# Optimization experiments

Measured on AMD Instinct MI355X. Metric: run time of the kernel, lower is better.

Reference implementation:

```python
import jax, jax.numpy as jnp
import numpy as np

N_NODES = 100_000
N_EDGES = 1_600_000
D_IN, D_H, D_OUT = 128, 128, 64


def setup_inputs() -> dict:
    key = jax.random.key(0)
    ks = jax.random.split(key, 8)
    x = jax.random.normal(ks[0], (N_NODES, D_IN), dtype=jnp.float32)
    edge_index = jax.random.randint(ks[1], (2, N_EDGES), 0, N_NODES, dtype=jnp.int32)
    def glorot(k, shape):
        lim = float(np.sqrt(6.0 / (shape[0] + shape[1])))
        return jax.random.uniform(k, shape, jnp.float32, -lim, lim)
    return {
        "x": x,
        "edge_index": edge_index,
        "W1": glorot(ks[2], (D_IN, D_H)),  "b1": jnp.zeros((D_H,), jnp.float32),
        "W2": glorot(ks[3], (D_H, D_H)),   "b2": jnp.zeros((D_H,), jnp.float32),
        "W3": glorot(ks[4], (D_H, D_OUT)), "b3": jnp.zeros((D_OUT,), jnp.float32),
    }


def gcn_conv(x, edge_index, W, b, num_nodes):
    # PyG GCNConv: add self-loops, symmetric D^-1/2 (A+I) D^-1/2 normalization,
    # linear transform before aggregation, then bias.
    xw = x @ W                                   # [N, D_out]
    loops = jnp.arange(num_nodes, dtype=edge_index.dtype)
    row = jnp.concatenate([edge_index[0], loops])  # source nodes
    col = jnp.concatenate([edge_index[1], loops])  # target nodes
    deg = jax.ops.segment_sum(jnp.ones_like(col, xw.dtype), col,
                              num_segments=num_nodes)
    dinv = jnp.where(deg > 0, jax.lax.rsqrt(jnp.maximum(deg, 1e-12)), 0.0)
    norm = dinv[row] * dinv[col]                 # [E+N]
    msg = xw[row] * norm[:, None]                # gather + scale
    out = jax.ops.segment_sum(msg, col, num_segments=num_nodes)
    return out + b


def reference(x, edge_index, W1, b1, W2, b2, W3, b3):
    # Dropout(0.2) is identity in eval/inference mode.
    h = jax.nn.relu(gcn_conv(x, edge_index, W1, b1, N_NODES))
    h = jax.nn.relu(gcn_conv(h, edge_index, W2, b2, N_NODES))
    return gcn_conv(h, edge_index, W3, b3, N_NODES)
```

## Files before the change

kernel.cpp:

```cpp
#include <hip/hip_runtime.h>

#define NN 100000
#define NE 1600000
constexpr int KDIM = 128;
constexpr int NPB = 128;
constexpr int G = (NN + NPB - 1) / NPB;
constexpr int CH = 4096;
constexpr int NCH = (NE + CH - 1) / CH;
constexpr int CAP = 4000;

typedef _Float16 f16x4 __attribute__((ext_vector_type(4)));
typedef _Float16 f16x8 __attribute__((ext_vector_type(8)));
typedef float f32x4 __attribute__((ext_vector_type(4)));
using half8 = f16x8;

__device__ __forceinline__ int swz(int byte) {
  return byte ^ (((byte >> 8) & 7) << 4);
}


__global__ __launch_bounds__(256) void k_zero(int* p, int n) {
  int i = blockIdx.x * 256 + threadIdx.x;
  if (i < n) p[i] = 0;
}

__global__ __launch_bounds__(256) void k_bucketP(const int* __restrict__ row,
                                                 const int* __restrict__ col,
                                                 int* __restrict__ cursor,
                                                 unsigned long long* __restrict__ temp) {
  __shared__ int h[G];
  for (int i = threadIdx.x; i < G; i += 256) h[i] = 0;
  __syncthreads();
  const int base = blockIdx.x * CH;
  const int m = min(CH, NE - base);
  for (int i = threadIdx.x; i < m; i += 256) atomicAdd(&h[col[base + i] >> 7], 1);
  __syncthreads();
  for (int i = threadIdx.x; i < G; i += 256) {
    int c = h[i];
    if (c) h[i] = atomicAdd(&cursor[i], c);
  }
  __syncthreads();
  for (int i = threadIdx.x; i < m; i += 256) {
    int cc = col[base + i];
    int rr = row[base + i];
    int slot = atomicAdd(&h[cc >> 7], 1);
    temp[(size_t)(cc >> 7) * CAP + slot] =
        ((unsigned long long)(unsigned)cc << 32) | (unsigned)rr;
  }
}

__global__ void k_bscan(const int* __restrict__ cnt, int* __restrict__ bbase) {
  __shared__ int sd[256];
  const int t = threadIdx.x;
  int v[4];
  int s = 0;
#pragma unroll
  for (int j = 0; j < 4; ++j) {
    int idx = t * 4 + j;
    v[j] = (idx < G) ? cnt[idx] : 0;
    s += v[j];
  }
  sd[t] = s;
  __syncthreads();
  for (int off = 1; off < 256; off <<= 1) {
    int x = (t >= off) ? sd[t - off] : 0;
    __syncthreads();
    sd[t] += x;
    __syncthreads();
  }
  int run = sd[t] - s;
#pragma unroll
  for (int j = 0; j < 4; ++j) {
    int idx = t * 4 + j;
    if (idx < G) bbase[idx] = run;
    run += v[j];
  }
  if (t == 255) bbase[G] = run;
}

__global__ __launch_bounds__(256) void k_groupP(const unsigned long long* __restrict__ temp,
                                                const int* __restrict__ bbase,
                                                int* __restrict__ rowptr,
                                                float* __restrict__ dinv,
                                                int* __restrict__ srcs) {
  __shared__ int fill[NPB];
  __shared__ int nbase[NPB];
  __shared__ int sc[NPB];
  const int g = blockIdx.x, t = threadIdx.x;
  const int lo = g * NPB;
  const int b0 = bbase[g];
  const int n = bbase[g + 1] - b0;
  const unsigned long long* tp = temp + (size_t)g * CAP;
  if (t < NPB) fill[t] = 0;
  __syncthreads();
  for (int s = t; s < n; s += 256) {
    int cc = (int)(tp[s] >> 32);
    atomicAdd(&fill[cc & (NPB - 1)], 1);
  }
  __syncthreads();
  int v = 0;
  if (t < NPB) {
    v = fill[t];
    sc[t] = v;
  }
  __syncthreads();
  for (int off = 1; off < NPB; off <<= 1) {
    int x = 0;
    if (t < NPB && t >= off) x = sc[t - off];
    __syncthreads();
    if (t < NPB) sc[t] += x;
    __syncthreads();
  }
  if (t < NPB) {
    int excl = sc[t] - v;
    nbase[t] = b0 + excl;
    int node = lo + t;
    if (node < NN) {
      rowptr[node] = b0 + excl;
      dinv[node] = rsqrtf((float)(v + 1));
    }
    fill[t] = 0;
  }
  if (g == G - 1 && t == 0) rowptr[NN] = NE;
  __syncthreads();
  for (int s = t; s < n; s += 256) {
    unsigned long long p = tp[s];
    int cc = (int)(p >> 32);
    int rr = (int)(unsigned)(p & 0xffffffffull);
    int c = cc & (NPB - 1);
    int slot = atomicAdd(&fill[c], 1);
    srcs[nbase[c] + slot] = rr;
  }
}

__global__ __launch_bounds__(256) void k_wconvAll(const float* __restrict__ W1,
                                                  const float* __restrict__ W2,
                                                  const float* __restrict__ W3,
                                                  _Float16* __restrict__ w1h,
                                                  _Float16* __restrict__ w2h,
                                                  _Float16* __restrict__ w3h) {
  int i = blockIdx.x * 256 + threadIdx.x;
  if (i < 16384) {
    int k = i >> 7, c = i & 127;
    w1h[c * 128 + k] = (_Float16)W1[i];
  } else if (i < 32768) {
    int j = i - 16384;
    int k = j >> 7, c = j & 127;
    w2h[c * 128 + k] = (_Float16)W2[j];
  } else if (i < 40960) {
    int j = i - 32768;
    int k = j >> 6, c = j & 63;
    w3h[c * 128 + k] = (_Float16)W3[j];
  }
}

template <int BN, bool F32IN>
__global__ __launch_bounds__(256, 2) void k_gemm_mfma(const void* __restrict__ Ain,
                                                      const _Float16* __restrict__ Wt_g,
                                                      const float* __restrict__ dinv,
                                                      _Float16* __restrict__ Y, int M) {
  constexpr int NB = BN / 16;
  __shared__ _Float16 Ah[128 * 128];
  __shared__ _Float16 Wt[BN * 128];
  const int t = threadIdx.x;
  const int rbase = blockIdx.x * 128;

  for (int c = t; c < BN * 16; c += 256) {
    f16x8 v = *(const f16x8*)((const char*)Wt_g + c * 16);
    *(f16x8*)((char*)Wt + swz(c * 16)) = v;
  }
  if constexpr (F32IN) {
    const float* A = (const float*)Ain;
    for (int c = t; c < 2048; c += 256) {
      int r = c >> 4, kc = c & 15;
      int row = rbase + r;
      f16x8 h = {};
      if (row < M) {
        float dv = dinv[row];
        const float* p = A + (size_t)row * 128 + kc * 8;
        float4 u0 = *(const float4*)p;
        float4 u1 = *(const float4*)(p + 4);
        h[0] = (_Float16)(u0.x * dv);
        h[1] = (_Float16)(u0.y * dv);
        h[2] = (_Float16)(u0.z * dv);
        h[3] = (_Float16)(u0.w * dv);
        h[4] = (_Float16)(u1.x * dv);
        h[5] = (_Float16)(u1.y * dv);
        h[6] = (_Float16)(u1.z * dv);
        h[7] = (_Float16)(u1.w * dv);
      }
      *(f16x8*)((char*)Ah + swz(c * 16)) = h;
    }
  } else {
    const _Float16* A = (const _Float16*)Ain;
    for (int c = t; c < 2048; c += 256) {
      int r = c >> 4;
      int row = rbase + r;
      f16x8 h = {};
      if (row < M) h = *(const f16x8*)(A + (size_t)row * 128 + (c & 15) * 8);
      *(f16x8*)((char*)Ah + swz(c * 16)) = h;
    }
  }
  __syncthreads();

  const int wave = t >> 6, lane = t & 63;
  const int l16 = lane & 15, lk = lane >> 4;

  f32x4 acc[2][NB];
#pragma unroll
  for (int mm = 0; mm < 2; ++mm)
#pragma unroll
    for (int n = 0; n < NB; ++n) acc[mm][n] = (f32x4){0.f, 0.f, 0.f, 0.f};

#pragma unroll
  for (int ks = 0; ks < 4; ++ks) {
    const int kbyte = ks * 64 + lk * 16;
    f16x8 afr[2];
#pragma unroll
    for (int mm = 0; mm < 2; ++mm) {
      int row = wave * 32 + mm * 16 + l16;
      afr[mm] = *(const f16x8*)((const char*)Ah + swz(row * 256 + kbyte));
    }
#pragma unroll
    for (int n = 0; n < NB; ++n) {
      int wrow = n * 16 + l16;
      f16x8 wfr = *(const f16x8*)((const char*)Wt + swz(wrow * 256 + kbyte));
#pragma unroll
      for (int mm = 0; mm < 2; ++mm)
        acc[mm][n] = __builtin_amdgcn_mfma_f32_16x16x32_f16(wfr, afr[mm], acc[mm][n], 0, 0, 0);
    }
  }

#pragma unroll
  for (int mm = 0; mm < 2; ++mm) {
    int row = rbase + wave * 32 + mm * 16 + l16;
    if (row < M) {
      _Float16* yr = Y + (size_t)row * BN + lk * 4;
#pragma unroll
      for (int n = 0; n < NB; ++n) {
        f16x4 h = {(_Float16)acc[mm][n][0], (_Float16)acc[mm][n][1],
                   (_Float16)acc[mm][n][2], (_Float16)acc[mm][n][3]};
        *(f16x4*)(yr + n * 16) = h;
      }
    } else if (row == M) {
      _Float16* yr = Y + (size_t)row * BN + lk * 4;
      f16x4 z = {};
#pragma unroll
      for (int n = 0; n < NB; ++n) *(f16x4*)(yr + n * 16) = z;
    }
  }
}

__global__ __launch_bounds__(256) void k_agg128h(const _Float16* __restrict__ Y,
                                                 const int* __restrict__ rowptr,
                                                 const int* __restrict__ srcs,
                                                 const float* __restrict__ dinv,
                                                 const float* __restrict__ bias,
                                                 _Float16* __restrict__ Out, int n) {
  const int wave = threadIdx.x >> 6;
  const int lane = threadIdx.x & 63;
  const int node = blockIdx.x * 4 + wave;
  if (node >= n) return;
  const int part = lane >> 4;
  const int q = lane & 15;
  const int jb = rowptr[node];
  const int je = rowptr[node + 1];

  float acc[8];
#pragma unroll
  for (int j = 0; j < 8; ++j) acc[j] = 0.f;
  {
    half8 s = *(const half8*)(Y + (size_t)node * 128 + q * 8);
    if (part == 0) {
#pragma unroll
      for (int j = 0; j < 8; ++j) acc[j] = (float)s[j];
    }
  }

  for (int j0 = jb; j0 < je; j0 += 64) {
    const int m = min(64, je - j0);
    const int idx = (lane < m) ? srcs[j0 + lane] : NN;
    for (int eb = 0; eb < m; eb += 32) {
      const int e0 = eb + part;
      int s0 = __shfl(idx, e0);
      int s1 = __shfl(idx, e0 + 4);
      int s2 = __shfl(idx, e0 + 8);
      int s3 = __shfl(idx, e0 + 12);
      int s4 = __shfl(idx, e0 + 16);
      int s5 = __shfl(idx, e0 + 20);
      int s6 = __shfl(idx, e0 + 24);
      int s7 = __shfl(idx, e0 + 28);
      half8 v0 = *(const half8*)(Y + (size_t)s0 * 128 + q * 8);
      half8 v1 = *(const half8*)(Y + (size_t)s1 * 128 + q * 8);
      half8 v2 = *(const half8*)(Y + (size_t)s2 * 128 + q * 8);
      half8 v3 = *(const half8*)(Y + (size_t)s3 * 128 + q * 8);
      half8 v4 = *(const half8*)(Y + (size_t)s4 * 128 + q * 8);
      half8 v5 = *(const half8*)(Y + (size_t)s5 * 128 + q * 8);
      half8 v6 = *(const half8*)(Y + (size_t)s6 * 128 + q * 8);
      half8 v7 = *(const half8*)(Y + (size_t)s7 * 128 + q * 8);
      half8 sA = (v0 + v1) + (v2 + v3);
      half8 sB = (v4 + v5) + (v6 + v7);
#pragma unroll
      for (int j = 0; j < 8; ++j) acc[j] += (float)sA[j];
#pragma unroll
      for (int j = 0; j < 8; ++j) acc[j] += (float)sB[j];
    }
  }

#pragma unroll
  for (int j = 0; j < 8; ++j) {
    acc[j] += __shfl_xor(acc[j], 16);
    acc[j] += __shfl_xor(acc[j], 32);
  }

  if (part == 0) {
    const float dv = dinv[node];
    f16x8 h;
#pragma unroll
    for (int j = 0; j < 8; ++j) {
      float o = fmaf(acc[j], dv, bias[q * 8 + j]);
      o = fmaxf(o, 0.f);
      h[j] = (_Float16)(o * dv);
    }
    *(f16x8*)(Out + (size_t)node * 128 + q * 8) = h;
  }
}

__global__ __launch_bounds__(256) void k_agg64h(const _Float16* __restrict__ Y,
                                                const int* __restrict__ rowptr,
                                                const int* __restrict__ srcs,
                                                const float* __restrict__ dinv,
                                                const float* __restrict__ bias,
                                                float* __restrict__ Out, int n) {
  const int wave = threadIdx.x >> 6;
  const int lane = threadIdx.x & 63;
  const int node = blockIdx.x * 4 + wave;
  if (node >= n) return;
  const int part = lane >> 3;
  const int q = lane & 7;
  const int jb = rowptr[node];
  const int je = rowptr[node + 1];

  float acc[8];
#pragma unroll
  for (int j = 0; j < 8; ++j) acc[j] = 0.f;
  {
    half8 s = *(const half8*)(Y + (size_t)node * 64 + q * 8);
    if (part == 0) {
#pragma unroll
      for (int j = 0; j < 8; ++j) acc[j] = (float)s[j];
    }
  }

  for (int j0 = jb; j0 < je; j0 += 64) {
    const int m = min(64, je - j0);
    const int idx = (lane < m) ? srcs[j0 + lane] : NN;
    const int e0 = part;
    int s0 = __shfl(idx, e0);
    int s1 = __shfl(idx, e0 + 8);
    int s2 = __shfl(idx, e0 + 16);
    int s3 = __shfl(idx, e0 + 24);
    int s4 = __shfl(idx, e0 + 32);
    int s5 = __shfl(idx, e0 + 40);
    int s6 = __shfl(idx, e0 + 48);
    int s7 = __shfl(idx, e0 + 56);
    half8 v0 = *(const half8*)(Y + (size_t)s0 * 64 + q * 8);
    half8 v1 = *(const half8*)(Y + (size_t)s1 * 64 + q * 8);
    half8 v2 = *(const half8*)(Y + (size_t)s2 * 64 + q * 8);
    half8 v3 = *(const half8*)(Y + (size_t)s3 * 64 + q * 8);
    half8 v4 = *(const half8*)(Y + (size_t)s4 * 64 + q * 8);
    half8 v5 = *(const half8*)(Y + (size_t)s5 * 64 + q * 8);
    half8 v6 = *(const half8*)(Y + (size_t)s6 * 64 + q * 8);
    half8 v7 = *(const half8*)(Y + (size_t)s7 * 64 + q * 8);
    half8 sA = (v0 + v1) + (v2 + v3);
    half8 sB = (v4 + v5) + (v6 + v7);
#pragma unroll
    for (int j = 0; j < 8; ++j) acc[j] += (float)sA[j];
#pragma unroll
    for (int j = 0; j < 8; ++j) acc[j] += (float)sB[j];
  }

#pragma unroll
  for (int j = 0; j < 8; ++j) {
    acc[j] += __shfl_xor(acc[j], 8);
    acc[j] += __shfl_xor(acc[j], 16);
    acc[j] += __shfl_xor(acc[j], 32);
  }

  if (part == 0) {
    const float dv = dinv[node];
    float o[8];
#pragma unroll
    for (int j = 0; j < 8; ++j) o[j] = fmaf(acc[j], dv, bias[q * 8 + j]);
    float* orow = Out + (size_t)node * 64 + q * 8;
    *(float4*)(orow) = make_float4(o[0], o[1], o[2], o[3]);
    *(float4*)(orow + 4) = make_float4(o[4], o[5], o[6], o[7]);
  }
}


extern "C" void kernel_launch(void* const* d_in, const int* in_sizes, int n_in,
                              void* d_out, int out_size, void* d_ws, size_t ws_size,
                              hipStream_t stream) {
  const float* x = (const float*)d_in[0];
  const int* ei = (const int*)d_in[1];
  const float* W1 = (const float*)d_in[2];
  const float* b1 = (const float*)d_in[3];
  const float* W2 = (const float*)d_in[4];
  const float* b2 = (const float*)d_in[5];
  const float* W3 = (const float*)d_in[6];
  const float* b3 = (const float*)d_in[7];
  float* out = (float*)d_out;

  const int* erow = ei;
  const int* ecol = ei + NE;

  char* w = (char*)d_ws;
  auto alloc = [&](size_t b) {
    char* p = w;
    w += (b + 255) & ~(size_t)255;
    return (void*)p;
  };
  float* dinv = (float*)alloc((size_t)NN * 4);
  int* rowptr = (int*)alloc((size_t)(NN + 1) * 4);
  int* cursor = (int*)alloc((size_t)G * 4);
  int* bbase = (int*)alloc((size_t)(G + 1) * 4);
  int* srcs = (int*)alloc((size_t)NE * 4);
  _Float16* w1h = (_Float16*)alloc((size_t)128 * 128 * 2);
  _Float16* w2h = (_Float16*)alloc((size_t)128 * 128 * 2);
  _Float16* w3h = (_Float16*)alloc((size_t)128 * 64 * 2);
  _Float16* ybuf = (_Float16*)alloc((size_t)(NN + 1) * 128 * 2);
  _Float16* hbuf = (_Float16*)alloc((size_t)(NN + 1) * 128 * 2);
  unsigned long long* temp = (unsigned long long*)ybuf;

  k_zero<<<(G + 255) / 256, 256, 0, stream>>>(cursor, G);
  k_bucketP<<<NCH, 256, 0, stream>>>(erow, ecol, cursor, temp);
  k_bscan<<<1, 256, 0, stream>>>(cursor, bbase);
  k_groupP<<<G, 256, 0, stream>>>(temp, bbase, rowptr, dinv, srcs);
  k_wconvAll<<<160, 256, 0, stream>>>(W1, W2, W3, w1h, w2h, w3h);

  const int nbG = (NN + 127) / 128;
  const int nbA = (NN + 3) / 4;

  k_gemm_mfma<128, true><<<nbG, 256, 0, stream>>>(x, w1h, dinv, ybuf, NN);
  k_agg128h<<<nbA, 256, 0, stream>>>(ybuf, rowptr, srcs, dinv, b1, hbuf, NN);
  k_gemm_mfma<128, false><<<nbG, 256, 0, stream>>>(hbuf, w2h, dinv, ybuf, NN);
  k_agg128h<<<nbA, 256, 0, stream>>>(ybuf, rowptr, srcs, dinv, b2, hbuf, NN);
  k_gemm_mfma<64, false><<<nbG, 256, 0, stream>>>(hbuf, w3h, dinv, ybuf, NN);
  k_agg64h<<<nbA, 256, 0, stream>>>(ybuf, rowptr, srcs, dinv, b3, out, NN);
}
```

Measured before the change: 279.1 us.

## Pack bucket entries to 32 bits, merge scan with weight convert, use global_load_lds

Bucket temp entries shrink from 64-bit (col,row) pairs to 32-bit words that pack a 7-bit local column with a 17-bit source row, halving scratch traffic in the bucket and group passes. The bucketing chunk size doubles. The bucket scan and the weight conversion now run in one launch instead of two. The GEMM loads W and full A tiles straight into LDS with global_load_lds, keeping the swizzle on the global side. The aggregation kernels load the self-loop row only in the lanes that use it.

```diff
diff --git a/kernel.cpp b/kernel.cpp
--- a/kernel.cpp
+++ b/kernel.cpp
@@ -5,10 +5,11 @@
 constexpr int KDIM = 128;
 constexpr int NPB = 128;
 constexpr int G = (NN + NPB - 1) / NPB;
-constexpr int CH = 4096;
+constexpr int CH = 8192;
 constexpr int NCH = (NE + CH - 1) / CH;
 constexpr int CAP = 4000;
 
+typedef unsigned int u32;
 typedef _Float16 f16x4 __attribute__((ext_vector_type(4)));
 typedef _Float16 f16x8 __attribute__((ext_vector_type(8)));
 typedef float f32x4 __attribute__((ext_vector_type(4)));
@@ -18,6 +19,12 @@
   return byte ^ (((byte >> 8) & 7) << 4);
 }
 
+__device__ __forceinline__ void gload16(const void* g, void* l) {
+  __builtin_amdgcn_global_load_lds(
+      (const __attribute__((address_space(1))) u32*)g,
+      (__attribute__((address_space(3))) u32*)l, 16, 0, 0);
+}
+
 
 __global__ __launch_bounds__(256) void k_zero(int* p, int n) {
   int i = blockIdx.x * 256 + threadIdx.x;
@@ -27,7 +34,7 @@
 __global__ __launch_bounds__(256) void k_bucketP(const int* __restrict__ row,
                                                  const int* __restrict__ col,
                                                  int* __restrict__ cursor,
-                                                 unsigned long long* __restrict__ temp) {
+                                                 u32* __restrict__ temp) {
   __shared__ int h[G];
   for (int i = threadIdx.x; i < G; i += 256) h[i] = 0;
   __syncthreads();
@@ -44,41 +51,63 @@
     int cc = col[base + i];
     int rr = row[base + i];
     int slot = atomicAdd(&h[cc >> 7], 1);
-    temp[(size_t)(cc >> 7) * CAP + slot] =
-        ((unsigned long long)(unsigned)cc << 32) | (unsigned)rr;
-  }
-}
-
-__global__ void k_bscan(const int* __restrict__ cnt, int* __restrict__ bbase) {
-  __shared__ int sd[256];
+    temp[(size_t)(cc >> 7) * CAP + slot] = ((u32)(cc & 127) << 17) | (u32)rr;
+  }
+}
+
+__global__ __launch_bounds__(256) void k_scan_wconv(const int* __restrict__ cnt,
+                                                    int* __restrict__ bbase,
+                                                    const float* __restrict__ W1,
+                                                    const float* __restrict__ W2,
+                                                    const float* __restrict__ W3,
+                                                    _Float16* __restrict__ w1h,
+                                                    _Float16* __restrict__ w2h,
+                                                    _Float16* __restrict__ w3h) {
   const int t = threadIdx.x;
-  int v[4];
-  int s = 0;
-#pragma unroll
-  for (int j = 0; j < 4; ++j) {
-    int idx = t * 4 + j;
-    v[j] = (idx < G) ? cnt[idx] : 0;
-    s += v[j];
-  }
-  sd[t] = s;
-  __syncthreads();
-  for (int off = 1; off < 256; off <<= 1) {
-    int x = (t >= off) ? sd[t - off] : 0;
+  if (blockIdx.x == 0) {
+    __shared__ int sd[256];
+    int v[4];
+    int s = 0;
+#pragma unroll
+    for (int j = 0; j < 4; ++j) {
+      int idx = t * 4 + j;
+      v[j] = (idx < G) ? cnt[idx] : 0;
+      s += v[j];
+    }
+    sd[t] = s;
     __syncthreads();
-    sd[t] += x;
-    __syncthreads();
-  }
-  int run = sd[t] - s;
-#pragma unroll
-  for (int j = 0; j < 4; ++j) {
-    int idx = t * 4 + j;
-    if (idx < G) bbase[idx] = run;
-    run += v[j];
-  }
-  if (t == 255) bbase[G] = run;
-}
-
-__global__ __launch_bounds__(256) void k_groupP(const unsigned long long* __restrict__ temp,
+    for (int off = 1; off < 256; off <<= 1) {
+      int x = (t >= off) ? sd[t - off] : 0;
+      __syncthreads();
+      sd[t] += x;
+      __syncthreads();
+    }
+    int run = sd[t] - s;
+#pragma unroll
+    for (int j = 0; j < 4; ++j) {
+      int idx = t * 4 + j;
+      if (idx < G) bbase[idx] = run;
+      run += v[j];
+    }
+    if (t == 255) bbase[G] = run;
+  } else {
+    int i = (blockIdx.x - 1) * 256 + t;
+    if (i < 16384) {
+      int k = i >> 7, c = i & 127;
+      w1h[c * 128 + k] = (_Float16)W1[i];
+    } else if (i < 32768) {
+      int j = i - 16384;
+      int k = j >> 7, c = j & 127;
+      w2h[c * 128 + k] = (_Float16)W2[j];
+    } else if (i < 40960) {
+      int j = i - 32768;
+      int k = j >> 6, c = j & 63;
+      w3h[c * 128 + k] = (_Float16)W3[j];
+    }
+  }
+}
+
+__global__ __launch_bounds__(256) void k_groupP(const u32* __restrict__ temp,
                                                 const int* __restrict__ bbase,
                                                 int* __restrict__ rowptr,
                                                 float* __restrict__ dinv,
@@ -90,13 +119,10 @@
   const int lo = g * NPB;
   const int b0 = bbase[g];
   const int n = bbase[g + 1] - b0;
-  const unsigned long long* tp = temp + (size_t)g * CAP;
+  const u32* tp = temp + (size_t)g * CAP;
   if (t < NPB) fill[t] = 0;
   __syncthreads();
-  for (int s = t; s < n; s += 256) {
-    int cc = (int)(tp[s] >> 32);
-    atomicAdd(&fill[cc & (NPB - 1)], 1);
-  }
+  for (int s = t; s < n; s += 256) atomicAdd(&fill[tp[s] >> 17], 1);
   __syncthreads();
   int v = 0;
   if (t < NPB) {
@@ -124,33 +150,10 @@
   if (g == G - 1 && t == 0) rowptr[NN] = NE;
   __syncthreads();
   for (int s = t; s < n; s += 256) {
-    unsigned long long p = tp[s];
-    int cc = (int)(p >> 32);
-    int rr = (int)(unsigned)(p & 0xffffffffull);
-    int c = cc & (NPB - 1);
+    u32 p = tp[s];
+    int c = p >> 17;
     int slot = atomicAdd(&fill[c], 1);
-    srcs[nbase[c] + slot] = rr;
-  }
-}
-
-__global__ __launch_bounds__(256) void k_wconvAll(const float* __restrict__ W1,
-                                                  const float* __restrict__ W2,
-                                                  const float* __restrict__ W3,
-                                                  _Float16* __restrict__ w1h,
-                                                  _Float16* __restrict__ w2h,
-                                                  _Float16* __restrict__ w3h) {
-  int i = blockIdx.x * 256 + threadIdx.x;
-  if (i < 16384) {
-    int k = i >> 7, c = i & 127;
-    w1h[c * 128 + k] = (_Float16)W1[i];
-  } else if (i < 32768) {
-    int j = i - 16384;
-    int k = j >> 7, c = j & 127;
-    w2h[c * 128 + k] = (_Float16)W2[j];
-  } else if (i < 40960) {
-    int j = i - 32768;
-    int k = j >> 6, c = j & 63;
-    w3h[c * 128 + k] = (_Float16)W3[j];
+    srcs[nbase[c] + slot] = (int)(p & 0x1FFFFu);
   }
 }
 
@@ -164,10 +167,15 @@
   __shared__ _Float16 Wt[BN * 128];
   const int t = threadIdx.x;
   const int rbase = blockIdx.x * 128;
-
-  for (int c = t; c < BN * 16; c += 256) {
-    f16x8 v = *(const f16x8*)((const char*)Wt_g + c * 16);
-    *(f16x8*)((char*)Wt + swz(c * 16)) = v;
+  const int wbase = (t & ~63) * 16;
+
+  {
+    const char* Wg = (const char*)Wt_g;
+    char* Wl = (char*)Wt;
+#pragma unroll
+    for (int c0 = 0; c0 < BN * 16; c0 += 256) {
+      gload16(Wg + swz((c0 + t) * 16), Wl + c0 * 16 + wbase);
+    }
   }
   if constexpr (F32IN) {
     const float* A = (const float*)Ain;
@@ -191,6 +199,13 @@
       }
       *(f16x8*)((char*)Ah + swz(c * 16)) = h;
     }
+  } else if (rbase + 128 <= M) {
+    const char* Ag = (const char*)Ain + (size_t)rbase * 256;
+    char* Al = (char*)Ah;
+#pragma unroll
+    for (int c0 = 0; c0 < 2048; c0 += 256) {
+      gload16(Ag + swz((c0 + t) * 16), Al + c0 * 16 + wbase);
+    }
   } else {
     const _Float16* A = (const _Float16*)Ain;
     for (int c = t; c < 2048; c += 256) {
@@ -269,12 +284,10 @@
   float acc[8];
 #pragma unroll
   for (int j = 0; j < 8; ++j) acc[j] = 0.f;
-  {
+  if (part == 0) {
     half8 s = *(const half8*)(Y + (size_t)node * 128 + q * 8);
-    if (part == 0) {
-#pragma unroll
-      for (int j = 0; j < 8; ++j) acc[j] = (float)s[j];
-    }
+#pragma unroll
+    for (int j = 0; j < 8; ++j) acc[j] = (float)s[j];
   }
 
   for (int j0 = jb; j0 < je; j0 += 64) {
@@ -344,12 +357,10 @@
   float acc[8];
 #pragma unroll
   for (int j = 0; j < 8; ++j) acc[j] = 0.f;
-  {
+  if (part == 0) {
     half8 s = *(const half8*)(Y + (size_t)node * 64 + q * 8);
-    if (part == 0) {
-#pragma unroll
-      for (int j = 0; j < 8; ++j) acc[j] = (float)s[j];
-    }
+#pragma unroll
+    for (int j = 0; j < 8; ++j) acc[j] = (float)s[j];
   }
 
   for (int j0 = jb; j0 < je; j0 += 64) {
@@ -431,13 +442,12 @@
   _Float16* w3h = (_Float16*)alloc((size_t)128 * 64 * 2);
   _Float16* ybuf = (_Float16*)alloc((size_t)(NN + 1) * 128 * 2);
   _Float16* hbuf = (_Float16*)alloc((size_t)(NN + 1) * 128 * 2);
-  unsigned long long* temp = (unsigned long long*)ybuf;
+  u32* temp = (u32*)ybuf;
 
   k_zero<<<(G + 255) / 256, 256, 0, stream>>>(cursor, G);
   k_bucketP<<<NCH, 256, 0, stream>>>(erow, ecol, cursor, temp);
-  k_bscan<<<1, 256, 0, stream>>>(cursor, bbase);
+  k_scan_wconv<<<161, 256, 0, stream>>>(cursor, bbase, W1, W2, W3, w1h, w2h, w3h);
   k_groupP<<<G, 256, 0, stream>>>(temp, bbase, rowptr, dinv, srcs);
-  k_wconvAll<<<160, 256, 0, stream>>>(W1, W2, W3, w1h, w2h, w3h);
 
   const int nbG = (NN + 127) / 128;
   const int nbA = (NN + 3) / 4;
```

Result: faster. 258.7 us (-7.3%).
